# Optimization experiments

Hardware: AMD Instinct MI355X
Metric: run time of the kernel (lower is better)

## Reference

```python
import jax, jax.numpy as jnp
import numpy as np
from functools import partial

# Module hyperparameters (from init_kwargs)
T, C_IN, H, W_DIM = 128, 16, 64, 64
C_OUT, KH, KW = 64, 3, 3
PAD = ((1, 1), (1, 1))  # (top,bottom),(left,right) -> symmetric here
STRIDES = (1, 1)
F_V_THRESH = 8.0
F_V_THRESH_LOW = -1.0
F_V_RESET = 0.0
# fVSubtract is None -> reset-to-value branch


def setup_inputs() -> dict:
    key = jax.random.key(0)
    kx, kw, kb = jax.random.split(key, 3)
    x = jax.random.uniform(kx, (T, C_IN, H, W_DIM), dtype=jnp.float32)
    fan_in = C_IN * KH * KW
    bound = 1.0 / np.sqrt(fan_in)
    W = jax.random.uniform(kw, (C_OUT, C_IN, KH, KW), dtype=jnp.float32,
                           minval=-bound, maxval=bound)
    b = jax.random.uniform(kb, (C_OUT,), dtype=jnp.float32,
                           minval=-bound, maxval=bound)
    return {"x": x, "W": W, "b": b}


def _spiking_conv(x, W, b):
    # conv over all timesteps at once (time is the conv batch dim): [T, C_out, H, W]
    conv_out = jax.lax.conv_general_dilated(
        x, W, window_strides=STRIDES, padding=PAD,
        dimension_numbers=("NCHW", "OIHW", "NCHW"))
    conv_out = conv_out + b[None, :, None, None]

    def step(state, conv_t):
        state = state + conv_t
        spikes = (state >= F_V_THRESH).astype(conv_t.dtype)
        # reset-to-value branch (fVSubtract is None)
        state = spikes * F_V_RESET + state * (1.0 - spikes)
        # nn.Threshold(v, v): x if x > v else v
        state = jnp.where(state > F_V_THRESH_LOW, state, F_V_THRESH_LOW)
        return state, spikes

    init_state = jnp.zeros(conv_out.shape[1:], dtype=conv_out.dtype)
    _, num_spikes = jax.lax.scan(step, init_state, conv_out)
    return num_spikes  # [T, C_out, H, W] float (0/1)


def reference(x, W, b):
    return _spiking_conv(x, W, b)
```

## Files before the change

kernel.cpp:

```cpp
#include <hip/hip_runtime.h>

#define T_STEPS 128
#define CIN     16
#define HH      64
#define WW      64
#define COUT    64
#define HWSZ    (HH * WW)
#define CHW     (COUT * HWSZ)
#define XCHW    (CIN * HWSZ)

#define TILE    32
#define HALO    34
#define LSTR    36
#define PLANE   (HALO * LSTR)
#define NST     (CIN * HALO * HALO)
#define WBLK    40

__global__ void transpose_w(const float* __restrict__ W, float* __restrict__ Wtr) {
    int e = blockIdx.x * 256 + threadIdx.x;
    if (e >= COUT * CIN * 9) return;
    int co = e / (CIN * 9);
    int r  = e - co * (CIN * 9);
    int ci = r / 9;
    int k  = r - ci * 9;
    Wtr[((co >> 2) * CIN + ci) * WBLK + (co & 3) * 9 + k] = W[e];
}

__global__ __launch_bounds__(512, 4)
void spiking_conv_pass1(const float* __restrict__ x, const float* __restrict__ Wtr,
                        const float* __restrict__ b, float* __restrict__ out) {
    __shared__ float xs[CIN * PLANE];

    const int tid  = threadIdx.x;
    const int t    = blockIdx.y;
    const int coh  = blockIdx.x & 1;
    const int tile = blockIdx.x >> 1;
    const int h0   = (tile >> 1) * TILE;
    const int w0   = (tile & 1) * TILE;

    const float* xt = x + t * XCHW;
    {
        float vbuf[19]; int ibuf[19];
#pragma unroll
        for (int k = 0; k < 18; ++k) {
            unsigned e = tid + k * 512;
            unsigned ci = e / (HALO * HALO);
            unsigned rem = e - ci * (HALO * HALO);
            unsigned r  = rem / HALO;
            unsigned c  = rem - r * HALO;
            int gh = h0 - 1 + (int)r;
            int gw = w0 - 1 + (int)c;
            bool inb = (unsigned)gh < HH && (unsigned)gw < WW;
            vbuf[k] = inb ? xt[ci * HWSZ + gh * WW + gw] : 0.f;
            ibuf[k] = ci * PLANE + r * LSTR + c;
        }
#pragma unroll
        for (int k = 0; k < 18; ++k) xs[ibuf[k]] = vbuf[k];
#pragma unroll
        for (int k = 0; k < 19; ++k) {
            unsigned e = tid + (18 + k) * 512;
            unsigned ci = e / (HALO * HALO);
            unsigned rem = e - ci * (HALO * HALO);
            unsigned r  = rem / HALO;
            unsigned c  = rem - r * HALO;
            int gh = h0 - 1 + (int)r;
            int gw = w0 - 1 + (int)c;
            bool inb = e < NST && (unsigned)gh < HH && (unsigned)gw < WW;
            vbuf[k] = inb ? xt[ci * HWSZ + gh * WW + gw] : 0.f;
            ibuf[k] = (e < NST) ? (int)(ci * PLANE + r * LSTR + c) : -1;
        }
#pragma unroll
        for (int k = 0; k < 19; ++k)
            if (ibuf[k] >= 0) xs[ibuf[k]] = vbuf[k];
    }
    __syncthreads();

    const int cog = __builtin_amdgcn_readfirstlane(tid >> 8);
    const int sp  = tid & 255;
    const int pr0 = sp >> 3;
    const int pc0 = (sp & 7) * 4;
    float* outt = out + t * CHW;

    float acc[16][4];
#pragma unroll
    for (int j = 0; j < 16; ++j)
#pragma unroll
        for (int p = 0; p < 4; ++p) acc[j][p] = 0.f;

#pragma unroll 1
    for (int ci = 0; ci < CIN; ++ci) {
        float xv[3][6];
#pragma unroll
        for (int dr = 0; dr < 3; ++dr) {
            const float* row = &xs[ci * PLANE + (pr0 + dr) * LSTR + pc0];
            float4 a  = *(const float4*)row;
            float2 c2 = *(const float2*)(row + 4);
            xv[dr][0] = a.x;  xv[dr][1] = a.y;
            xv[dr][2] = a.z;  xv[dr][3] = a.w;
            xv[dr][4] = c2.x; xv[dr][5] = c2.y;
        }
#pragma unroll
        for (int g = 0; g < 4; ++g) {
            const int g4 = coh * 8 + cog * 4 + g;
            const float* wb = Wtr + (g4 * CIN + ci) * WBLK;
            float w[36];
#pragma unroll
            for (int i = 0; i < 36; ++i) w[i] = wb[i];
#pragma unroll
            for (int jj = 0; jj < 4; ++jj)
#pragma unroll
                for (int ky = 0; ky < 3; ++ky)
#pragma unroll
                    for (int kx = 0; kx < 3; ++kx) {
                        const float wv = w[jj * 9 + ky * 3 + kx];
#pragma unroll
                        for (int p = 0; p < 4; ++p)
                            acc[g * 4 + jj][p] += wv * xv[ky][kx + p];
                    }
        }
    }

#pragma unroll
    for (int g = 0; g < 4; ++g)
#pragma unroll
        for (int jj = 0; jj < 4; ++jj) {
            const int co = coh * 32 + cog * 16 + g * 4 + jj;
            const float bias = b[co];
            float4 o;
            o.x = acc[g * 4 + jj][0] + bias;
            o.y = acc[g * 4 + jj][1] + bias;
            o.z = acc[g * 4 + jj][2] + bias;
            o.w = acc[g * 4 + jj][3] + bias;
            *(float4*)&outt[co * HWSZ + (h0 + pr0) * WW + (w0 + pc0)] = o;
        }
}

#define SCH 128

__device__ __forceinline__ void gl_lds_4(const float* g, float* l) {
    __builtin_amdgcn_global_load_lds(
        (const __attribute__((address_space(1))) void*)g,
        (__attribute__((address_space(3))) void*)l, 4, 0, 0);
}

__global__ __launch_bounds__(256)
void spiking_scan_pass2(float* __restrict__ io) {
    __shared__ float tile[T_STEPS * SCH];
    const int tid = threadIdx.x;
    const int wv  = tid >> 6;
    const int ln  = tid & 63;
    const int s0  = blockIdx.x * SCH;

#pragma unroll
    for (int i = 0; i < 32; ++i) {
        const int t = wv * 32 + i;
        const float* g = io + t * CHW + s0;
        float* l = &tile[t * SCH];
        gl_lds_4(g + ln, l);
        gl_lds_4(g + 64 + ln, l + 64);
    }
    __syncthreads();

    if (tid < SCH) {
        float s = 0.f;
#pragma unroll 8
        for (int t = 0; t < T_STEPS; ++t) {
            float v = tile[t * SCH + tid];
            s += v;
            const bool sp = (s >= 8.0f);
            tile[t * SCH + tid] = sp ? 1.0f : 0.0f;
            s = sp ? 0.0f : s;
            s = fmaxf(s, -1.0f);
        }
    }
    __syncthreads();

#pragma unroll
    for (int i = 0; i < 32; ++i) {
        const int t = wv * 32 + i;
        float2 v = *(const float2*)&tile[t * SCH + ln * 2];
        *(float2*)(io + t * CHW + s0 + ln * 2) = v;
    }
}

extern "C" void kernel_launch(void* const* d_in, const int* in_sizes, int n_in,
                              void* d_out, int out_size, void* d_ws, size_t ws_size,
                              hipStream_t stream) {
    const float* x = (const float*)d_in[0];
    const float* W = (const float*)d_in[1];
    const float* b = (const float*)d_in[2];
    float* out = (float*)d_out;
    float* Wtr = (float*)d_ws;

    transpose_w<<<36, 256, 0, stream>>>(W, Wtr);

    dim3 g1(8, 128);
    spiking_conv_pass1<<<g1, 512, 0, stream>>>(x, Wtr, b, out);

    spiking_scan_pass2<<<CHW / SCH, 256, 0, stream>>>(out);
}
```

Measured before the change: 267.4 us.

## Chunk spiking scan over time and reverse conv time order for L2 reuse

Reverses the time order of conv blocks so the earliest timesteps are written last and are likely still cached when the scan starts. Splits the scan into four sequential launches of 32 timesteps each, carrying membrane state in a global workspace buffer. Each scan block now uses all 256 threads over 256 positions with wider 16-byte LDS loads and float4 stores, giving higher occupancy from smaller shared tiles. This costs extra kernel launches and state reads and writes per chunk.

Measured after the change: 275.8 us. 1.03x slower.

```diff
diff --git a/kernel.cpp b/kernel.cpp
--- a/kernel.cpp
+++ b/kernel.cpp
@@ -32,7 +32,7 @@
     __shared__ float xs[CIN * PLANE];
 
     const int tid  = threadIdx.x;
-    const int t    = blockIdx.y;
+    const int t    = 127 - blockIdx.y;
     const int coh  = blockIdx.x & 1;
     const int tile = blockIdx.x >> 1;
     const int h0   = (tile >> 1) * TILE;
@@ -135,51 +135,47 @@
         }
 }
 
-#define SCH 128
-
-__device__ __forceinline__ void gl_lds_4(const float* g, float* l) {
-    __builtin_amdgcn_global_load_lds(
-        (const __attribute__((address_space(1))) void*)g,
-        (__attribute__((address_space(3))) void*)l, 4, 0, 0);
-}
+#define SCH 256
+#define TCK 32
 
 __global__ __launch_bounds__(256)
-void spiking_scan_pass2(float* __restrict__ io) {
-    __shared__ float tile[T_STEPS * SCH];
-    const int tid = threadIdx.x;
-    const int wv  = tid >> 6;
-    const int ln  = tid & 63;
-    const int s0  = blockIdx.x * SCH;
+void spiking_scan_chunk(float* __restrict__ io, float* __restrict__ state,
+                        int t0) {
+    __shared__ float tile[TCK][SCH];
+    const int tid  = threadIdx.x;
+    const int wv   = tid >> 6;
+    const int ln   = tid & 63;
+    const int base = blockIdx.x * SCH;
 
 #pragma unroll
-    for (int i = 0; i < 32; ++i) {
-        const int t = wv * 32 + i;
-        const float* g = io + t * CHW + s0;
-        float* l = &tile[t * SCH];
-        gl_lds_4(g + ln, l);
-        gl_lds_4(g + 64 + ln, l + 64);
+    for (int i = 0; i < 8; ++i) {
+        const int r = wv * 8 + i;
+        const float* g = io + (size_t)(t0 + r) * CHW + base;
+        __builtin_amdgcn_global_load_lds(
+            (const __attribute__((address_space(1))) void*)(g + ln * 4),
+            (__attribute__((address_space(3))) void*)&tile[r][0], 16, 0, 0);
     }
     __syncthreads();
 
-    if (tid < SCH) {
-        float s = 0.f;
-#pragma unroll 8
-        for (int t = 0; t < T_STEPS; ++t) {
-            float v = tile[t * SCH + tid];
-            s += v;
-            const bool sp = (s >= 8.0f);
-            tile[t * SCH + tid] = sp ? 1.0f : 0.0f;
-            s = sp ? 0.0f : s;
-            s = fmaxf(s, -1.0f);
-        }
+    float s = 0.f;
+    if (t0 != 0) s = state[base + tid];
+#pragma unroll
+    for (int r = 0; r < TCK; ++r) {
+        float v = tile[r][tid];
+        s += v;
+        const bool sp = (s >= 8.0f);
+        tile[r][tid] = sp ? 1.0f : 0.0f;
+        s = sp ? 0.0f : s;
+        s = fmaxf(s, -1.0f);
     }
+    state[base + tid] = s;
     __syncthreads();
 
 #pragma unroll
-    for (int i = 0; i < 32; ++i) {
-        const int t = wv * 32 + i;
-        float2 v = *(const float2*)&tile[t * SCH + ln * 2];
-        *(float2*)(io + t * CHW + s0 + ln * 2) = v;
+    for (int i = 0; i < 8; ++i) {
+        const int r = wv * 8 + i;
+        float4 v = *(const float4*)&tile[r][ln * 4];
+        *(float4*)(io + (size_t)(t0 + r) * CHW + base + ln * 4) = v;
     }
 }
 
@@ -190,12 +186,14 @@
     const float* W = (const float*)d_in[1];
     const float* b = (const float*)d_in[2];
     float* out = (float*)d_out;
-    float* Wtr = (float*)d_ws;
+    float* Wtr   = (float*)d_ws;
+    float* state = (float*)((char*)d_ws + 65536);
 
     transpose_w<<<36, 256, 0, stream>>>(W, Wtr);
 
     dim3 g1(8, 128);
     spiking_conv_pass1<<<g1, 512, 0, stream>>>(x, Wtr, b, out);
 
-    spiking_scan_pass2<<<CHW / SCH, 256, 0, stream>>>(out);
+    for (int c = 0; c < T_STEPS / TCK; ++c)
+        spiking_scan_chunk<<<CHW / SCH, 256, 0, stream>>>(out, state, c * TCK);
 }
```
